# Kernel optimization log

Measured on AMD Instinct MI355X. Metric: run time of the kernel, lower is better.

## Reference

```python
import jax, jax.numpy as jnp
import numpy as np

IN_FEATURES = 4096
OUT_FEATURES = 4096
MAX_RANK = 32
ALPHA = 32
SCALING = ALPHA / MAX_RANK  # 1.0


def setup_inputs() -> dict:
    key = jax.random.key(0)
    k_x, k_u, k_v = jax.random.split(key, 3)
    x = jax.random.normal(k_x, (4, 2048, IN_FEATURES), dtype=jnp.float32)
    U = jax.random.normal(k_u, (OUT_FEATURES, MAX_RANK), dtype=jnp.float32) * 0.01
    S = jnp.ones((MAX_RANK,), dtype=jnp.float32)
    V = jax.random.normal(k_v, (MAX_RANK, IN_FEATURES), dtype=jnp.float32) * 0.01
    return {"x": x, "U": U, "S": S, "V": V}


def reference(x, U, S, V):
    # Original: W = U @ diag(S) @ V ; out = (x @ W.T) * scaling  (dropout=0 -> Identity)
    # Mathematically identical factored form: ((x @ V^T) * S) @ U^T * scaling.
    h = jnp.einsum('bsi,ri->bsr', x, V)        # [B,S,rank]
    h = h * S                                   # scale by singular values
    out = jnp.einsum('bsr,or->bso', h, U)       # [B,S,out]
    return out * SCALING
```

## Files before the change

kernel.cpp:

```cpp
#include <hip/hip_runtime.h>
#include <hip/hip_bf16.h>

typedef __bf16 bf16x4 __attribute__((ext_vector_type(4)));
typedef __bf16 bf16x8 __attribute__((ext_vector_type(8)));
typedef float  f32x4  __attribute__((ext_vector_type(4)));

#define IN_F   4096
#define OUT_F  4096
#define RANK   32

__device__ __forceinline__ bf16x8 cvt8(float4 a, float4 b) {
    bf16x8 r;
    r[0] = (__bf16)a.x; r[1] = (__bf16)a.y; r[2] = (__bf16)a.z; r[3] = (__bf16)a.w;
    r[4] = (__bf16)b.x; r[5] = (__bf16)b.y; r[6] = (__bf16)b.z; r[7] = (__bf16)b.w;
    return r;
}
__device__ __forceinline__ bf16x4 cvt4(float4 a) {
    bf16x4 r;
    r[0] = (__bf16)a.x; r[1] = (__bf16)a.y; r[2] = (__bf16)a.z; r[3] = (__bf16)a.w;
    return r;
}

__global__ __launch_bounds__(256, 8)
void lora_h(const float* __restrict__ X, const float* __restrict__ V,
            __hip_bfloat16* __restrict__ Hpart)
{
    __shared__ __bf16 XL[2][32 * 64];
    __shared__ __bf16 VL[2][32 * 64];

    const int tid  = threadIdx.x;
    const int wave = tid >> 6;
    const int lane = tid & 63;
    const int r    = lane & 15;
    const int kg   = lane >> 4;

    const int tt = wave & 1;
    const int rh = wave >> 1;

    const int t0 = blockIdx.x * 32;
    const int f0 = blockIdx.y * 512;

    auto stage = [&](int c, int buf) {
        const int fc = f0 + c * 64;
        #pragma unroll
        for (int i = 0; i < 2; ++i) {
            const int f4   = tid + i * 256;
            const int row  = f4 >> 4;
            const int colf = (f4 & 15) * 4;
            float4 xv = *reinterpret_cast<const float4*>(
                X + (size_t)(t0 + row) * IN_F + fc + colf);
            float4 vv = *reinterpret_cast<const float4*>(
                V + (size_t)row * IN_F + fc + colf);
            const int e = colf ^ ((row & 7) << 3);
            *reinterpret_cast<bf16x4*>(&XL[buf][row * 64 + e]) = cvt4(xv);
            *reinterpret_cast<bf16x4*>(&VL[buf][row * 64 + e]) = cvt4(vv);
        }
    };

    f32x4 acc = {0.f, 0.f, 0.f, 0.f};

    auto compute = [&](int buf) {
        const int sw = (r & 7) << 3;
        #pragma unroll
        for (int s = 0; s < 2; ++s) {
            bf16x8 xb = *reinterpret_cast<const bf16x8*>(
                &XL[buf][(tt * 16 + r) * 64 + ((s * 32 + kg * 8) ^ sw)]);
            bf16x8 vb = *reinterpret_cast<const bf16x8*>(
                &VL[buf][(rh * 16 + r) * 64 + ((s * 32 + kg * 8) ^ sw)]);
            acc = __builtin_amdgcn_mfma_f32_16x16x32_bf16(xb, vb, acc, 0, 0, 0);
        }
    };

    stage(0, 0);
    __syncthreads();

    for (int c = 0; c < 8; ++c) {
        if (c + 1 < 8) stage(c + 1, (c + 1) & 1);
        compute(c & 1);
        __syncthreads();
    }

    __hip_bfloat16* Hq = Hpart + (size_t)blockIdx.y * (8192 * RANK)
                               + (size_t)(t0 + tt * 16) * RANK;
    #pragma unroll
    for (int j = 0; j < 4; ++j)
        Hq[(size_t)(kg * 4 + j) * RANK + rh * 16 + r] = (__hip_bfloat16)acc[j];
}

template <int NKS>
__global__ __launch_bounds__(256)
void lora_hred(const ushort* __restrict__ Hpart, const float* __restrict__ S,
               float* __restrict__ H)
{
    const int idx = (blockIdx.x * 256 + threadIdx.x) * 4;
    const int rk  = idx & 31;

    float acc[4] = {0.f, 0.f, 0.f, 0.f};
    #pragma unroll
    for (int k = 0; k < NKS; ++k) {
        ushort4 u = *reinterpret_cast<const ushort4*>(
            Hpart + (size_t)k * (8192 * RANK) + idx);
        acc[0] += __uint_as_float((unsigned)u.x << 16);
        acc[1] += __uint_as_float((unsigned)u.y << 16);
        acc[2] += __uint_as_float((unsigned)u.z << 16);
        acc[3] += __uint_as_float((unsigned)u.w << 16);
    }
    float4 out;
    out.x = acc[0] * S[rk];
    out.y = acc[1] * S[rk + 1];
    out.z = acc[2] * S[rk + 2];
    out.w = acc[3] * S[rk + 3];
    *reinterpret_cast<float4*>(H + idx) = out;
}

__global__ __launch_bounds__(256)
void lora_h_naive(const float* __restrict__ X, const float* __restrict__ S,
                  const float* __restrict__ V, float* __restrict__ H)
{
    const int idx = blockIdx.x * 256 + threadIdx.x;
    const int tok = idx >> 5, rk = idx & 31;
    float acc = 0.f;
    for (int f = 0; f < IN_F; ++f)
        acc += X[(size_t)tok * IN_F + f] * V[(size_t)rk * IN_F + f];
    H[idx] = acc * S[rk];
}

__global__ __launch_bounds__(256, 4)
void lora_out(const float* __restrict__ H, const float* __restrict__ U,
              float* __restrict__ Out)
{
    __shared__ float Hs[32][33];

    const int tid  = threadIdx.x;
    const int wave = tid >> 6;
    const int lane = tid & 63;
    const int r    = lane & 15;
    const int kg   = lane >> 4;

    const int tt = blockIdx.x >> 2;
    const int cq = blockIdx.x & 3;
    const int t0 = tt * 32;

    {
        float4 v = reinterpret_cast<const float4*>(H + (size_t)t0 * RANK)[tid];
        const int tok = tid >> 3;
        const int rr  = (tid & 7) * 4;
        Hs[tok][rr] = v.x; Hs[tok][rr + 1] = v.y;
        Hs[tok][rr + 2] = v.z; Hs[tok][rr + 3] = v.w;
    }
    __syncthreads();

    bf16x8 hb[2];
    #pragma unroll
    for (int a = 0; a < 2; ++a)
        #pragma unroll
        for (int j = 0; j < 8; ++j) hb[a][j] = (__bf16)Hs[a * 16 + r][kg * 8 + j];

    const int wc0 = cq * 1024 + wave * 256;

    #pragma unroll
    for (int g = 0; g < 4; ++g) {
        float4 u0[4], u1[4];
        #pragma unroll
        for (int b = 0; b < 4; ++b) {
            const float4* up = reinterpret_cast<const float4*>(
                U + (size_t)(wc0 + g * 64 + b * 16 + r) * RANK + kg * 8);
            u0[b] = up[0];
            u1[b] = up[1];
        }
        #pragma unroll
        for (int b = 0; b < 4; ++b) {
            bf16x8 ub = cvt8(u0[b], u1[b]);
            #pragma unroll
            for (int a = 0; a < 2; ++a) {
                f32x4 d = {0.f, 0.f, 0.f, 0.f};
                d = __builtin_amdgcn_mfma_f32_16x16x32_bf16(ub, hb[a], d, 0, 0, 0);
                *reinterpret_cast<float4*>(
                    Out + (size_t)(t0 + a * 16 + r) * OUT_F
                        + wc0 + g * 64 + b * 16 + kg * 4)
                    = *reinterpret_cast<float4*>(&d);
            }
        }
    }
}

extern "C" void kernel_launch(void* const* d_in, const int* in_sizes, int n_in,
                              void* d_out, int out_size, void* d_ws, size_t ws_size,
                              hipStream_t stream) {
    const float* X = (const float*)d_in[0];
    const float* U = (const float*)d_in[1];
    const float* S = (const float*)d_in[2];
    const float* V = (const float*)d_in[3];
    float* Out = (float*)d_out;

    float* H = (float*)d_ws;
    __hip_bfloat16* Hpart = (__hip_bfloat16*)((float*)d_ws + 262144);

    if (ws_size >= (size_t)5 * 1024 * 1024) {
        lora_h<<<dim3(256, 8), 256, 0, stream>>>(X, V, Hpart);
        lora_hred<8><<<256, 256, 0, stream>>>((const ushort*)Hpart, S, H);
        lora_out<<<1024, 256, 0, stream>>>(H, U, Out);
    } else {
        lora_h_naive<<<1024, 256, 0, stream>>>(X, S, V, H);
        lora_out<<<1024, 256, 0, stream>>>(H, U, Out);
    }
}
```

Measured before the change: 64.60 us.

## Fuse split-K reduction into output GEMM and retile H kernel to 64 tokens

The down-projection kernel now tiles 64 tokens by 32 ranks per block with a 16-way split over features. Each wave reuses its X fragment across both rank halves, and the starting chunk is staggered per block. The separate reduction kernel is removed: the output kernel sums the 16 bf16 partials and applies S while loading H into shared memory, which saves a launch and an fp32 H round-trip. The cost is that each output block re-reads 16 partials (4 column blocks read the same tokens), and the extra split slices double the partial-buffer traffic.

```diff
diff --git a/kernel.cpp b/kernel.cpp
--- a/kernel.cpp
+++ b/kernel.cpp
@@ -21,12 +21,91 @@
     return r;
 }
 
-__global__ __launch_bounds__(256, 8)
+template <int KS>
+__global__ __launch_bounds__(256, 6)
 void lora_h(const float* __restrict__ X, const float* __restrict__ V,
             __hip_bfloat16* __restrict__ Hpart)
 {
-    __shared__ __bf16 XL[2][32 * 64];
+    constexpr int SL   = IN_F / KS;
+    constexpr int NCHK = SL / 64;
+
+    __shared__ __bf16 XL[2][64 * 64];
     __shared__ __bf16 VL[2][32 * 64];
+
+    const int tid  = threadIdx.x;
+    const int tt   = tid >> 6;
+    const int lane = tid & 63;
+    const int r    = lane & 15;
+    const int kg   = lane >> 4;
+
+    const int t0 = blockIdx.x * 64;
+    const int f0 = blockIdx.y * SL;
+
+    auto stage = [&](int c, int buf) {
+        const int fc = f0 + ((c + blockIdx.x) & (NCHK - 1)) * 64;
+        #pragma unroll
+        for (int i = 0; i < 4; ++i) {
+            const int f4   = tid + i * 256;
+            const int row  = f4 >> 4;
+            const int colf = (f4 & 15) * 4;
+            float4 xv = *reinterpret_cast<const float4*>(
+                X + (size_t)(t0 + row) * IN_F + fc + colf);
+            *reinterpret_cast<bf16x4*>(
+                &XL[buf][row * 64 + (colf ^ ((row & 7) << 3))]) = cvt4(xv);
+        }
+        #pragma unroll
+        for (int i = 0; i < 2; ++i) {
+            const int f4   = tid + i * 256;
+            const int row  = f4 >> 4;
+            const int colf = (f4 & 15) * 4;
+            float4 vv = *reinterpret_cast<const float4*>(
+                V + (size_t)row * IN_F + fc + colf);
+            *reinterpret_cast<bf16x4*>(
+                &VL[buf][row * 64 + (colf ^ ((row & 7) << 3))]) = cvt4(vv);
+        }
+    };
+
+    f32x4 acc[2] = {};
+
+    auto compute = [&](int buf) {
+        const int sw = (r & 7) << 3;
+        #pragma unroll
+        for (int s = 0; s < 2; ++s) {
+            bf16x8 xb = *reinterpret_cast<const bf16x8*>(
+                &XL[buf][(tt * 16 + r) * 64 + ((s * 32 + kg * 8) ^ sw)]);
+            #pragma unroll
+            for (int rh = 0; rh < 2; ++rh) {
+                bf16x8 vb = *reinterpret_cast<const bf16x8*>(
+                    &VL[buf][(rh * 16 + r) * 64 + ((s * 32 + kg * 8) ^ sw)]);
+                acc[rh] = __builtin_amdgcn_mfma_f32_16x16x32_bf16(xb, vb, acc[rh], 0, 0, 0);
+            }
+        }
+    };
+
+    stage(0, 0);
+    __syncthreads();
+
+    for (int c = 0; c < NCHK; ++c) {
+        if (c + 1 < NCHK) stage(c + 1, (c + 1) & 1);
+        compute(c & 1);
+        __syncthreads();
+    }
+
+    __hip_bfloat16* Hq = Hpart + (size_t)blockIdx.y * (8192 * RANK)
+                               + (size_t)(t0 + tt * 16) * RANK;
+    #pragma unroll
+    for (int j = 0; j < 4; ++j) {
+        Hq[(size_t)(kg * 4 + j) * RANK + r]      = (__hip_bfloat16)acc[0][j];
+        Hq[(size_t)(kg * 4 + j) * RANK + 16 + r] = (__hip_bfloat16)acc[1][j];
+    }
+}
+
+template <int NKS>
+__global__ __launch_bounds__(256, 4)
+void lora_out_f(const ushort* __restrict__ Hpart, const float* __restrict__ S,
+                const float* __restrict__ U, float* __restrict__ Out)
+{
+    __shared__ float Hs[32][33];
 
     const int tid  = threadIdx.x;
     const int wave = tid >> 6;
@@ -34,119 +113,27 @@
     const int r    = lane & 15;
     const int kg   = lane >> 4;
 
-    const int tt = wave & 1;
-    const int rh = wave >> 1;
-
-    const int t0 = blockIdx.x * 32;
-    const int f0 = blockIdx.y * 512;
-
-    auto stage = [&](int c, int buf) {
-        const int fc = f0 + c * 64;
-        #pragma unroll
-        for (int i = 0; i < 2; ++i) {
-            const int f4   = tid + i * 256;
-            const int row  = f4 >> 4;
-            const int colf = (f4 & 15) * 4;
-            float4 xv = *reinterpret_cast<const float4*>(
-                X + (size_t)(t0 + row) * IN_F + fc + colf);
-            float4 vv = *reinterpret_cast<const float4*>(
-                V + (size_t)row * IN_F + fc + colf);
-            const int e = colf ^ ((row & 7) << 3);
-            *reinterpret_cast<bf16x4*>(&XL[buf][row * 64 + e]) = cvt4(xv);
-            *reinterpret_cast<bf16x4*>(&VL[buf][row * 64 + e]) = cvt4(vv);
-        }
-    };
-
-    f32x4 acc = {0.f, 0.f, 0.f, 0.f};
-
-    auto compute = [&](int buf) {
-        const int sw = (r & 7) << 3;
-        #pragma unroll
-        for (int s = 0; s < 2; ++s) {
-            bf16x8 xb = *reinterpret_cast<const bf16x8*>(
-                &XL[buf][(tt * 16 + r) * 64 + ((s * 32 + kg * 8) ^ sw)]);
-            bf16x8 vb = *reinterpret_cast<const bf16x8*>(
-                &VL[buf][(rh * 16 + r) * 64 + ((s * 32 + kg * 8) ^ sw)]);
-            acc = __builtin_amdgcn_mfma_f32_16x16x32_bf16(xb, vb, acc, 0, 0, 0);
-        }
-    };
-
-    stage(0, 0);
-    __syncthreads();
-
-    for (int c = 0; c < 8; ++c) {
-        if (c + 1 < 8) stage(c + 1, (c + 1) & 1);
-        compute(c & 1);
-        __syncthreads();
-    }
-
-    __hip_bfloat16* Hq = Hpart + (size_t)blockIdx.y * (8192 * RANK)
-                               + (size_t)(t0 + tt * 16) * RANK;
-    #pragma unroll
-    for (int j = 0; j < 4; ++j)
-        Hq[(size_t)(kg * 4 + j) * RANK + rh * 16 + r] = (__hip_bfloat16)acc[j];
-}
-
-template <int NKS>
-__global__ __launch_bounds__(256)
-void lora_hred(const ushort* __restrict__ Hpart, const float* __restrict__ S,
-               float* __restrict__ H)
-{
-    const int idx = (blockIdx.x * 256 + threadIdx.x) * 4;
-    const int rk  = idx & 31;
-
-    float acc[4] = {0.f, 0.f, 0.f, 0.f};
-    #pragma unroll
-    for (int k = 0; k < NKS; ++k) {
-        ushort4 u = *reinterpret_cast<const ushort4*>(
-            Hpart + (size_t)k * (8192 * RANK) + idx);
-        acc[0] += __uint_as_float((unsigned)u.x << 16);
-        acc[1] += __uint_as_float((unsigned)u.y << 16);
-        acc[2] += __uint_as_float((unsigned)u.z << 16);
-        acc[3] += __uint_as_float((unsigned)u.w << 16);
-    }
-    float4 out;
-    out.x = acc[0] * S[rk];
-    out.y = acc[1] * S[rk + 1];
-    out.z = acc[2] * S[rk + 2];
-    out.w = acc[3] * S[rk + 3];
-    *reinterpret_cast<float4*>(H + idx) = out;
-}
-
-__global__ __launch_bounds__(256)
-void lora_h_naive(const float* __restrict__ X, const float* __restrict__ S,
-                  const float* __restrict__ V, float* __restrict__ H)
-{
-    const int idx = blockIdx.x * 256 + threadIdx.x;
-    const int tok = idx >> 5, rk = idx & 31;
-    float acc = 0.f;
-    for (int f = 0; f < IN_F; ++f)
-        acc += X[(size_t)tok * IN_F + f] * V[(size_t)rk * IN_F + f];
-    H[idx] = acc * S[rk];
-}
-
-__global__ __launch_bounds__(256, 4)
-void lora_out(const float* __restrict__ H, const float* __restrict__ U,
-              float* __restrict__ Out)
-{
-    __shared__ float Hs[32][33];
-
-    const int tid  = threadIdx.x;
-    const int wave = tid >> 6;
-    const int lane = tid & 63;
-    const int r    = lane & 15;
-    const int kg   = lane >> 4;
-
     const int tt = blockIdx.x >> 2;
     const int cq = blockIdx.x & 3;
     const int t0 = tt * 32;
 
     {
-        float4 v = reinterpret_cast<const float4*>(H + (size_t)t0 * RANK)[tid];
+        const int rk = (tid & 7) * 4;
+        float a0 = 0.f, a1 = 0.f, a2 = 0.f, a3 = 0.f;
+        #pragma unroll
+        for (int k = 0; k < NKS; ++k) {
+            ushort4 u = *reinterpret_cast<const ushort4*>(
+                Hpart + (size_t)k * (8192 * RANK) + (size_t)t0 * RANK + tid * 4);
+            a0 += __uint_as_float((unsigned)u.x << 16);
+            a1 += __uint_as_float((unsigned)u.y << 16);
+            a2 += __uint_as_float((unsigned)u.z << 16);
+            a3 += __uint_as_float((unsigned)u.w << 16);
+        }
         const int tok = tid >> 3;
-        const int rr  = (tid & 7) * 4;
-        Hs[tok][rr] = v.x; Hs[tok][rr + 1] = v.y;
-        Hs[tok][rr + 2] = v.z; Hs[tok][rr + 3] = v.w;
+        Hs[tok][rk]     = a0 * S[rk];
+        Hs[tok][rk + 1] = a1 * S[rk + 1];
+        Hs[tok][rk + 2] = a2 * S[rk + 2];
+        Hs[tok][rk + 3] = a3 * S[rk + 3];
     }
     __syncthreads();
 
@@ -184,6 +171,88 @@
     }
 }
 
+template <int NKS>
+__global__ __launch_bounds__(256)
+void lora_hred(const ushort* __restrict__ Hpart, const float* __restrict__ S,
+               float* __restrict__ H)
+{
+    const int idx = (blockIdx.x * 256 + threadIdx.x) * 4;
+    const int rk  = idx & 31;
+    float acc[4] = {0.f, 0.f, 0.f, 0.f};
+    #pragma unroll
+    for (int k = 0; k < NKS; ++k) {
+        ushort4 u = *reinterpret_cast<const ushort4*>(
+            Hpart + (size_t)k * (8192 * RANK) + idx);
+        acc[0] += __uint_as_float((unsigned)u.x << 16);
+        acc[1] += __uint_as_float((unsigned)u.y << 16);
+        acc[2] += __uint_as_float((unsigned)u.z << 16);
+        acc[3] += __uint_as_float((unsigned)u.w << 16);
+    }
+    float4 out;
+    out.x = acc[0] * S[rk];     out.y = acc[1] * S[rk + 1];
+    out.z = acc[2] * S[rk + 2]; out.w = acc[3] * S[rk + 3];
+    *reinterpret_cast<float4*>(H + idx) = out;
+}
+
+__global__ __launch_bounds__(256, 4)
+void lora_out_h(const float* __restrict__ H, const float* __restrict__ U,
+                float* __restrict__ Out)
+{
+    __shared__ float Hs[32][33];
+
+    const int tid  = threadIdx.x;
+    const int wave = tid >> 6;
+    const int lane = tid & 63;
+    const int r    = lane & 15;
+    const int kg   = lane >> 4;
+
+    const int tt = blockIdx.x >> 2;
+    const int cq = blockIdx.x & 3;
+    const int t0 = tt * 32;
+
+    {
+        float4 v = reinterpret_cast<const float4*>(H + (size_t)t0 * RANK)[tid];
+        const int tok = tid >> 3;
+        const int rr  = (tid & 7) * 4;
+        Hs[tok][rr] = v.x; Hs[tok][rr + 1] = v.y;
+        Hs[tok][rr + 2] = v.z; Hs[tok][rr + 3] = v.w;
+    }
+    __syncthreads();
+
+    bf16x8 hb[2];
+    #pragma unroll
+    for (int a = 0; a < 2; ++a)
+        #pragma unroll
+        for (int j = 0; j < 8; ++j) hb[a][j] = (__bf16)Hs[a * 16 + r][kg * 8 + j];
+
+    const int wc0 = cq * 1024 + wave * 256;
+
+    #pragma unroll
+    for (int g = 0; g < 4; ++g) {
+        float4 u0[4], u1[4];
+        #pragma unroll
+        for (int b = 0; b < 4; ++b) {
+            const float4* up = reinterpret_cast<const float4*>(
+                U + (size_t)(wc0 + g * 64 + b * 16 + r) * RANK + kg * 8);
+            u0[b] = up[0];
+            u1[b] = up[1];
+        }
+        #pragma unroll
+        for (int b = 0; b < 4; ++b) {
+            bf16x8 ub = cvt8(u0[b], u1[b]);
+            #pragma unroll
+            for (int a = 0; a < 2; ++a) {
+                f32x4 d = {0.f, 0.f, 0.f, 0.f};
+                d = __builtin_amdgcn_mfma_f32_16x16x32_bf16(ub, hb[a], d, 0, 0, 0);
+                *reinterpret_cast<float4*>(
+                    Out + (size_t)(t0 + a * 16 + r) * OUT_F
+                        + wc0 + g * 64 + b * 16 + kg * 4)
+                    = *reinterpret_cast<float4*>(&d);
+            }
+        }
+    }
+}
+
 extern "C" void kernel_launch(void* const* d_in, const int* in_sizes, int n_in,
                               void* d_out, int out_size, void* d_ws, size_t ws_size,
                               hipStream_t stream) {
@@ -193,15 +262,15 @@
     const float* V = (const float*)d_in[3];
     float* Out = (float*)d_out;
 
-    float* H = (float*)d_ws;
-    __hip_bfloat16* Hpart = (__hip_bfloat16*)((float*)d_ws + 262144);
-
-    if (ws_size >= (size_t)5 * 1024 * 1024) {
-        lora_h<<<dim3(256, 8), 256, 0, stream>>>(X, V, Hpart);
-        lora_hred<8><<<256, 256, 0, stream>>>((const ushort*)Hpart, S, H);
-        lora_out<<<1024, 256, 0, stream>>>(H, U, Out);
+    if (ws_size >= (size_t)9 * 1024 * 1024) {
+        __hip_bfloat16* Hpart = (__hip_bfloat16*)d_ws;
+        lora_h<16><<<dim3(128, 16), 256, 0, stream>>>(X, V, Hpart);
+        lora_out_f<16><<<1024, 256, 0, stream>>>((const ushort*)Hpart, S, U, Out);
     } else {
-        lora_h_naive<<<1024, 256, 0, stream>>>(X, S, V, H);
-        lora_out<<<1024, 256, 0, stream>>>(H, U, Out);
-    }
-}
+        __hip_bfloat16* Hpart = (__hip_bfloat16*)d_out;
+        float* H = (float*)d_ws;
+        lora_h<16><<<dim3(128, 16), 256, 0, stream>>>(X, V, Hpart);
+        lora_hred<16><<<256, 256, 0, stream>>>((const ushort*)Hpart, S, H);
+        lora_out_h<<<1024, 256, 0, stream>>>(H, U, Out);
+    }
+}
```

Result: slower. 66.52 us (+3.0%).
